# Kernel optimization log

Measured on AMD Instinct MI355X. Metric: run time of the kernel, lower is better.

The kernel has to match this reference:

```python
import jax, jax.numpy as jnp
import numpy as np

G = (1.0, 1.0)  # metric signature, n_blades = 4

def to_hypercomplex(x, n_blades):
    # (..., n_blades*C) -> (..., C, n_blades)
    return x.reshape(*x.shape[:-1], n_blades, -1).swapaxes(-2, -1)

def clifford_kernel_2d(w, g):
    # w: (4, out, in) -> kernel (4*out, 4*in), cliffordlayers get_2d_clifford_kernel
    g0, g1 = g
    k0 = jnp.concatenate([w[0],  g0 * w[1],  g1 * w[2], -g0 * g1 * w[3]], axis=1)
    k1 = jnp.concatenate([w[1],  w[0],      -g1 * w[3],  g1 * w[2]], axis=1)
    k2 = jnp.concatenate([w[2],  g0 * w[3],  w[0],      -g0 * w[1]], axis=1)
    k3 = jnp.concatenate([w[3],  w[2],       w[1],       w[0]], axis=1)
    return jnp.concatenate([k0, k1, k2, k3], axis=0)

def clifford_linear(x, w, b, g=G):
    # x: (N, C_in, 4) ; w: (4, C_out, C_in) ; b: (4, C_out)
    N = x.shape[0]
    k = clifford_kernel_2d(w, g)                      # (4*C_out, 4*C_in)
    xf = x.swapaxes(-2, -1).reshape(N, -1)            # blade-major flatten (N, 4*C_in)
    out = xf @ k.T + b.reshape(-1)                    # (N, 4*C_out)
    C_out = w.shape[1]
    return out.reshape(N, 4, C_out).swapaxes(-2, -1)  # (N, C_out, 4)

def setup_inputs() -> dict:
    key = jax.random.key(0)
    ks = jax.random.split(key, 10)
    N, E, R, emb_dim = 100000, 600000, 500, 256
    C = emb_dim // 4
    s = 0.05
    return {
        "h": jax.random.normal(ks[0], (N, emb_dim), jnp.float32),
        "edge_index": jax.random.randint(ks[1], (2, E), 0, N, jnp.int64),
        "edge_type": jax.random.randint(ks[2], (E,), 0, R, jnp.int64),
        "relation_emb": jax.random.normal(ks[3], (R, emb_dim), jnp.float32),
        "msg_w": jax.random.normal(ks[4], (4, C, C), jnp.float32) * s,
        "msg_b": jax.random.normal(ks[5], (4, C), jnp.float32) * s,
        "upd_w": jax.random.normal(ks[6], (4, C, C), jnp.float32) * s,
        "upd_b": jax.random.normal(ks[7], (4, C), jnp.float32) * s,
        "gate_w": jax.random.normal(ks[8], (1, emb_dim), jnp.float32) * s,
        "gate_b": jax.random.normal(ks[9], (1,), jnp.float32) * s,
    }

def reference(h, edge_index, edge_type, relation_emb, msg_w, msg_b, upd_w, upd_b, gate_w, gate_b):
    n_blades = 4
    num_nodes = h.shape[0]
    h_hc = to_hypercomplex(h, n_blades)               # (N, C, 4)
    r_hc = to_hypercomplex(relation_emb, n_blades)    # (R, C, 4)
    src, dst = edge_index[0], edge_index[1]
    h_src = h_hc[src]                                 # (E, C, 4)
    r_uv = r_hc[edge_type]                            # (E, C, 4)
    m = clifford_linear(h_src * r_uv, msg_w, msg_b)   # (E, C, 4)
    gate = jax.nn.sigmoid(r_uv.reshape(r_uv.shape[0], -1) @ gate_w.T + gate_b)  # (E, 1)
    m = m * gate[:, :, None]
    ones = jnp.ones_like(src, dtype=jnp.float32)
    deg_src = jax.ops.segment_sum(ones, src, num_segments=num_nodes)
    deg_dst = jax.ops.segment_sum(ones, dst, num_segments=num_nodes)
    norm = jnp.maximum(deg_src[src] * deg_dst[dst], 1.0) ** -0.5
    m = m * norm[:, None, None]
    h_agg = jax.ops.segment_sum(m, dst, num_segments=num_nodes)  # (N, C, 4)
    h_out = clifford_linear(h_hc + h_agg, upd_w, upd_b)          # (N, C, 4)
    return h_out.reshape(num_nodes, -1)
```

## Files before the change

### kernel.cpp

```cpp
#include <hip/hip_runtime.h>
#include <math.h>

typedef unsigned int u32;
typedef unsigned short u16;
typedef __attribute__((ext_vector_type(8))) short bf16x8;
typedef __attribute__((ext_vector_type(4))) float f32x4;

__device__ inline u16 f2bf(float x) {
    union { float f; u32 u; } v; v.f = x;
    u32 r = v.u + 0x7FFFu + ((v.u >> 16) & 1u);
    return (u16)(r >> 16);
}
__device__ inline float bf2f(u16 x) { return __uint_as_float((u32)x << 16); }
__device__ inline float bf_lo(u32 u) { return __uint_as_float(u << 16); }
__device__ inline float bf_hi(u32 u) { return __uint_as_float(u & 0xffff0000u); }

__device__ __forceinline__ int cs_s(int ob, int ib) { return ob ^ ib; }
__device__ __forceinline__ float cs_g(int ob, int ib) {
    return ((ob != 3) && (ib == (3 ^ (ob & 1)))) ? -1.f : 1.f;
}

#define CAP 32


template <int BF>
__global__ __launch_bounds__(256) void prepC_kernel(
    const float* __restrict__ msg_w, const float* __restrict__ upd_w,
    const float* __restrict__ upd_b, const float* __restrict__ msg_b,
    const float* __restrict__ rel_emb, const float* __restrict__ gate_w,
    const float* __restrict__ gate_b, const float* __restrict__ h,
    const int* __restrict__ ei, const int* __restrict__ et, int E,
    u32* __restrict__ deg_src, u32* __restrict__ cursor,
    u32* __restrict__ bucket,
    float* __restrict__ gate, u16* __restrict__ Kcomb,
    float* __restrict__ c0, float* __restrict__ c1,
    u16* __restrict__ h_bf, u16* __restrict__ rel_bf,
    int N, int R, int nbDeg, int nbGate, int nbRel, int nbH) {
    __shared__ __align__(16) u16 ms[16384];
    __shared__ float U_s[256];
    __shared__ float wred[4];
    int tid = threadIdx.x;
    int idx = blockIdx.x >> 1;

    if (blockIdx.x & 1) {
        if (idx < 256) {
            int p = idx;
            int j = (p & 3) * 64 + (p >> 2);
#pragma unroll
            for (int i = 0; i < 8; ++i) {
                int c8 = i * 256 + tid;
                const float* p8 = msg_w + (size_t)c8 * 8;
                float4 a = *(const float4*)(p8);
                float4 bb = *(const float4*)(p8 + 4);
                u16 tmp[8] = {f2bf(a.x), f2bf(a.y), f2bf(a.z), f2bf(a.w),
                              f2bf(bb.x), f2bf(bb.y), f2bf(bb.z), f2bf(bb.w)};
                *(uint4*)&ms[c8 * 8] = *(const uint4*)tmp;
            }
            int ib = tid >> 6, ic = tid & 63;
            {
                int obu = j >> 6;
                U_s[tid] = cs_g(obu, ib) * upd_w[cs_s(obu, ib) * 4096 + (j & 63) * 64 + ic];
            }
            __syncthreads();
            float acc = 0.f;
#pragma unroll
            for (int ob = 0; ob < 4; ++ob) {
                int s = cs_s(ob, ib);
                float gg = cs_g(ob, ib);
                const u16* mp = ms + s * 4096 + ic;
                const float* us = U_s + ob * 64;
                float a0 = 0.f;
#pragma unroll 8
                for (int oc = 0; oc < 64; ++oc) a0 += us[oc] * bf2f(mp[oc * 64]);
                acc += gg * a0;
            }
            u16 vA = f2bf(acc);
            u16 vU = f2bf(U_s[tid]);
            int pt = p >> 4, pl = p & 15;
            int kgA = (tid >> 3) & 3, elA = tid & 7;
            size_t addrA = (size_t)(pt * 16 + (tid >> 5)) * 512 + (kgA * 16 + pl) * 8 + elA;
            int ku = tid + 256;
            size_t addrU = (size_t)(pt * 16 + (ku >> 5)) * 512 + (kgA * 16 + pl) * 8 + elA;
#pragma unroll
            for (int r = 0; r < 8; ++r) {
                Kcomb[(size_t)r * 131072 + addrA] = vA;
                Kcomb[(size_t)r * 131072 + addrU] = vU;
            }
            float part = U_s[tid] * msg_b[tid];
            int lane = tid & 63, wv = tid >> 6;
#pragma unroll
            for (int d = 32; d > 0; d >>= 1) part += __shfl_down(part, d);
            if (lane == 0) wred[wv] = part;
            __syncthreads();
            if (tid == 0) { c1[p] = wred[0] + wred[1] + wred[2] + wred[3]; c0[p] = upd_b[j]; }
            return;
        }
        int gb = idx - 256;
        if (gb < nbGate) {
            int wv = tid >> 6, lane = tid & 63;
            int r = gb * 4 + wv;
            if (r >= R) return;
            float4 rv = *(const float4*)(rel_emb + (size_t)r * 256 + lane * 4);
            float s = 0.f;
            float rvv[4] = {rv.x, rv.y, rv.z, rv.w};
#pragma unroll
            for (int c = 0; c < 4; ++c) {
                int jj = lane * 4 + c;
                s += rvv[c] * gate_w[(jj & 63) * 4 + (jj >> 6)];
            }
#pragma unroll
            for (int d = 32; d > 0; d >>= 1) s += __shfl_down(s, d);
            if (lane == 0) gate[r] = 1.0f / (1.0f + expf(-(s + gate_b[0])));
            return;
        }
        int rb = gb - nbGate;
        if (BF && rb < nbRel) {
            int i = rb * 256 + tid;
            if (i < R * 32) {
                const float* p8 = rel_emb + (size_t)i * 8;
                float4 a = *(const float4*)(p8);
                float4 bb = *(const float4*)(p8 + 4);
                u16 tmp[8] = {f2bf(a.x), f2bf(a.y), f2bf(a.z), f2bf(a.w),
                              f2bf(bb.x), f2bf(bb.y), f2bf(bb.z), f2bf(bb.w)};
                *(uint4*)(rel_bf + (size_t)i * 8) = *(const uint4*)tmp;
            }
            return;
        }
        int hb = rb - nbRel;
        if (BF && hb < nbH) {
            int n8 = N * 32;
            for (int i = hb * 256 + tid; i < n8; i += nbH * 256) {
                const float* p8 = h + (size_t)i * 8;
                float4 a = *(const float4*)(p8);
                float4 bb = *(const float4*)(p8 + 4);
                u16 tmp[8] = {f2bf(a.x), f2bf(a.y), f2bf(a.z), f2bf(a.w),
                              f2bf(bb.x), f2bf(bb.y), f2bf(bb.z), f2bf(bb.w)};
                *(uint4*)(h_bf + (size_t)i * 8) = *(const uint4*)tmp;
            }
        }
        return;
    }
    if (idx < nbDeg) {
        int e = idx * 256 + tid;
        if (e < E) {
            int src = ei[e];
            int dst = ei[E + e];
            int rel = et[e];
            atomicAdd(&deg_src[src], 1u);
            u32 pos = atomicAdd(&cursor[dst], 1u);
            if (pos < CAP)
                bucket[(size_t)dst * CAP + pos] = (u32)src | ((u32)rel << 18);
        }
    }
}

template <int BF>
__global__ __launch_bounds__(256, 4) void aggemm_kernel(
    float* __restrict__ dio,
    const float* __restrict__ h, const u16* __restrict__ h_bf,
    const float* __restrict__ rel_emb, const u16* __restrict__ rel_bf,
    const u16* __restrict__ Kcomb,
    const u32* __restrict__ cursor, const u32* __restrict__ deg_src,
    const u32* __restrict__ bucket, const float* __restrict__ gate,
    const float* __restrict__ c0, const float* __restrict__ c1, int N) {
    __shared__ __align__(16) u16 xs[32 * 512];
    __shared__ float ws_l[32];
    const int lane = threadIdx.x & 63;
    const int wv = threadIdx.x >> 6;
    const int l15 = lane & 15;
    const int kg = lane >> 4;
    const int half = lane >> 5, l32 = lane & 31;
    const int m0 = blockIdx.x * 32;
    const int pbase = wv * 64;
    const int pt0 = wv * 4;
    const u16* Kr = Kcomb + (size_t)(blockIdx.x & 7) * 131072;

    u32 ns4[4];
    float ddf4[4];
    u32 ent4[4];
    uint4 hrow4[4];
#pragma unroll
    for (int rnd = 0; rnd < 4; ++rnd) {
        int m = wv * 8 + rnd * 2 + half;
        int n = m0 + m;
        bool valid = n < N;
        u32 dd = valid ? cursor[n] : 0u;
        ns4[rnd] = dd < CAP ? dd : CAP;
        ddf4[rnd] = (float)dd;
        ent4[rnd] = (valid && l32 < (int)ns4[rnd])
                        ? bucket[(size_t)n * CAP + l32] : 0u;
        uint4 hr = make_uint4(0u, 0u, 0u, 0u);
        if (valid) {
            if (BF) {
                hr = *(const uint4*)(h_bf + (size_t)n * 256 + l32 * 8);
            } else {
                const float* hp = h + (size_t)n * 256 + l32 * 8;
                float4 f0 = *(const float4*)hp, f1 = *(const float4*)(hp + 4);
                u16 tmp[8] = {f2bf(f0.x), f2bf(f0.y), f2bf(f0.z), f2bf(f0.w),
                              f2bf(f1.x), f2bf(f1.y), f2bf(f1.z), f2bf(f1.w)};
                hr = *(const uint4*)tmp;
            }
        }
        hrow4[rnd] = hr;
    }

    float w4[4];
#pragma unroll
    for (int rnd = 0; rnd < 4; ++rnd) {
        float wl = 0.f;
        if (l32 < (int)ns4[rnd]) {
            u32 src_l = ent4[rnd] & 0x3FFFFu, rel_l = ent4[rnd] >> 18;
            float ds = (float)deg_src[src_l];
            wl = gate[rel_l] * rsqrtf(fmaxf(ds * ddf4[rnd], 1.0f));
        }
        w4[rnd] = wl;
    }

#pragma unroll
    for (int rnd = 0; rnd < 4; ++rnd) {
        int m = wv * 8 + rnd * 2 + half;
        u32 ns = ns4[rnd];
        int swm = (m & 7) << 3;
        u32 ent_l = ent4[rnd];
        float w_l = w4[rnd];

        float acc[8];
#pragma unroll
        for (int j = 0; j < 8; ++j) acc[j] = 0.f;
        float wsum = 0.f;

        for (u32 e = 0; e < ns; e += 4) {
            u32 ent[4];
            float wq[4];
            uint4 hv[4], rv[4];
#pragma unroll
            for (int q = 0; q < 4; ++q) {
                u32 idxq = e + q;
                u32 cl = (idxq < ns) ? idxq : (ns - 1);
                ent[q] = __shfl(ent_l, (int)cl, 32);
                float wv_ = __shfl(w_l, (int)cl, 32);
                wq[q] = (idxq < ns) ? wv_ : 0.f;
            }
#pragma unroll
            for (int q = 0; q < 4; ++q) {
                u32 src = ent[q] & 0x3FFFFu, rel = ent[q] >> 18;
                if (BF) {
                    hv[q] = *(const uint4*)(h_bf + (size_t)src * 256 + l32 * 8);
                    rv[q] = *(const uint4*)(rel_bf + (size_t)rel * 256 + l32 * 8);
                } else {
                    const float* hp = h + (size_t)src * 256 + l32 * 8;
                    const float* rp = rel_emb + (size_t)rel * 256 + l32 * 8;
                    float4 hf0 = *(const float4*)hp, hf1 = *(const float4*)(hp + 4);
                    float4 rf0 = *(const float4*)rp, rf1 = *(const float4*)(rp + 4);
                    u16 th[8] = {f2bf(hf0.x), f2bf(hf0.y), f2bf(hf0.z), f2bf(hf0.w),
                                 f2bf(hf1.x), f2bf(hf1.y), f2bf(hf1.z), f2bf(hf1.w)};
                    u16 tr[8] = {f2bf(rf0.x), f2bf(rf0.y), f2bf(rf0.z), f2bf(rf0.w),
                                 f2bf(rf1.x), f2bf(rf1.y), f2bf(rf1.z), f2bf(rf1.w)};
                    hv[q] = *(const uint4*)th;
                    rv[q] = *(const uint4*)tr;
                }
            }
#pragma unroll
            for (int q = 0; q < 4; ++q) {
                float w = wq[q];
                u32 hu[4] = {hv[q].x, hv[q].y, hv[q].z, hv[q].w};
                u32 ru[4] = {rv[q].x, rv[q].y, rv[q].z, rv[q].w};
#pragma unroll
                for (int c = 0; c < 4; ++c) {
                    acc[c * 2 + 0] += w * bf_lo(hu[c]) * bf_lo(ru[c]);
                    acc[c * 2 + 1] += w * bf_hi(hu[c]) * bf_hi(ru[c]);
                }
                wsum += w;
            }
        }

        u32 outw[4];
#pragma unroll
        for (int c = 0; c < 4; ++c)
            outw[c] = (u32)f2bf(acc[c * 2]) | ((u32)f2bf(acc[c * 2 + 1]) << 16);
        *(uint4*)&xs[m * 512 + ((l32 * 8) ^ swm)] = *(const uint4*)outw;
        *(uint4*)&xs[m * 512 + ((256 + l32 * 8) ^ swm)] = hrow4[rnd];
        if (l32 == 0) ws_l[m] = wsum;
    }
    __syncthreads();

    f32x4 acc[2][4];
#pragma unroll
    for (int f = 0; f < 2; ++f)
#pragma unroll
        for (int nf = 0; nf < 4; ++nf) acc[f][nf] = (f32x4)(0.f);

    const int swz = (l15 & 7) << 3;
#pragma unroll 4
    for (int k0 = 0; k0 < 512; k0 += 32) {
        int kk = k0 + kg * 8;
        int ksi = k0 >> 5;
        bf16x8 a[2], b[4];
#pragma unroll
        for (int f = 0; f < 2; ++f)
            a[f] = *(const bf16x8*)&xs[(f * 16 + l15) * 512 + (kk ^ swz)];
#pragma unroll
        for (int nf = 0; nf < 4; ++nf)
            b[nf] = *(const bf16x8*)(Kr + (size_t)((pt0 + nf) * 16 + ksi) * 512 + lane * 8);
#pragma unroll
        for (int f = 0; f < 2; ++f)
#pragma unroll
            for (int nf = 0; nf < 4; ++nf)
                acc[f][nf] = __builtin_amdgcn_mfma_f32_16x16x32_bf16(a[f], b[nf], acc[f][nf], 0, 0, 0);
    }

    float b0[4], b1[4];
#pragma unroll
    for (int nf = 0; nf < 4; ++nf) {
        int p = pbase + nf * 16 + l15;
        b0[nf] = c0[p];
        b1[nf] = c1[p];
    }
#pragma unroll
    for (int f = 0; f < 2; ++f) {
#pragma unroll
        for (int r = 0; r < 4; ++r) {
            int m = f * 16 + kg * 4 + r;
            int row = m0 + m;
            if (row >= N) continue;
            float wsv = ws_l[m];
#pragma unroll
            for (int nf = 0; nf < 4; ++nf) {
                int p = pbase + nf * 16 + l15;
                dio[(size_t)row * 256 + p] = acc[f][nf][r] + b0[nf] + b1[nf] * wsv;
            }
        }
    }
}

static inline size_t align4(size_t x) { return (x + 3) & ~(size_t)3; }
static inline int imax(int a, int b) { return a > b ? a : b; }

extern "C" void kernel_launch(void* const* d_in, const int* in_sizes, int n_in,
                              void* d_out, int out_size, void* d_ws, size_t ws_size,
                              hipStream_t stream) {
    const float* h       = (const float*)d_in[0];
    const int*   ei      = (const int*)d_in[1];
    const int*   et      = (const int*)d_in[2];
    const float* rel_emb = (const float*)d_in[3];
    const float* msg_w   = (const float*)d_in[4];
    const float* msg_b   = (const float*)d_in[5];
    const float* upd_w   = (const float*)d_in[6];
    const float* upd_b   = (const float*)d_in[7];
    const float* gate_w  = (const float*)d_in[8];
    const float* gate_b  = (const float*)d_in[9];

    const int N = in_sizes[0] / 256;
    const int E = in_sizes[2];
    const int R = in_sizes[3] / 256;

    u32* ws = (u32*)d_ws;
    size_t o = 0;
    u32* deg_src  = ws + o; o += align4((size_t)N);
    u32* cursor   = ws + o; o += align4((size_t)N);
    float* gate   = (float*)(ws + o); o += align4((size_t)R);
    u32* bucket   = ws + o; o += (size_t)align4((size_t)N) * CAP;
    u16* Kcomb    = (u16*)(ws + o); o += 524288;
    float* c0     = (float*)(ws + o); o += 256;
    float* c1     = (float*)(ws + o); o += 256;
    size_t need_base = o;
    u16* h_bf     = (u16*)(ws + o); o += (size_t)N * 128;
    u16* rel_bf   = (u16*)(ws + o); o += (size_t)R * 128;
    size_t need_bf = o;

    if (ws_size < need_base * 4) return;
    const bool use_bf = (ws_size >= need_bf * 4);

    float* out = (float*)d_out;

    hipMemsetAsync(deg_src, 0, 2 * align4((size_t)N) * 4, stream);

    const int nbDeg  = (E + 255) / 256;
    const int nbGate = (R + 3) / 4;
    const int nbRel  = use_bf ? (R * 32 + 255) / 256 : 0;
    const int nbH    = use_bf ? imax(256, nbDeg - 256 - nbGate - nbRel) : 0;
    const int gridC  = 2 * imax(nbDeg, 256 + nbGate + nbRel + nbH);
    if (use_bf) {
        prepC_kernel<1><<<gridC, 256, 0, stream>>>(
            msg_w, upd_w, upd_b, msg_b, rel_emb, gate_w, gate_b, h, ei, et, E,
            deg_src, cursor, bucket, gate, Kcomb, c0, c1, h_bf, rel_bf,
            N, R, nbDeg, nbGate, nbRel, nbH);
        aggemm_kernel<1><<<(N + 31) / 32, 256, 0, stream>>>(
            out, h, h_bf, rel_emb, rel_bf, Kcomb, cursor, deg_src, bucket, gate,
            c0, c1, N);
    } else {
        prepC_kernel<0><<<gridC, 256, 0, stream>>>(
            msg_w, upd_w, upd_b, msg_b, rel_emb, gate_w, gate_b, h, ei, et, E,
            deg_src, cursor, bucket, gate, Kcomb, c0, c1, h_bf, rel_bf,
            N, R, nbDeg, nbGate, nbRel, nbH);
        aggemm_kernel<0><<<(N + 31) / 32, 256, 0, stream>>>(
            out, h, h_bf, rel_emb, rel_bf, Kcomb, cursor, deg_src, bucket, gate,
            c0, c1, N);
    }
}
```

Baseline: 177.1 us.

## Load self-node A operand directly from global, halving shared staging

Stops staging each node's own h row in shared memory alongside the aggregated messages. The second half of the K loop now reads the h operand straight from global memory (bf16 or converted from fp32) into MFMA registers. This halves the LDS buffer and drops the hrow registers, and the occupancy target is raised from 4 to 6 blocks per CU. In exchange, every wave reloads the h rows from global/L2 instead of sharing one LDS copy, and the 6-wave launch bound may squeeze registers.

```diff
diff --git a/kernel.cpp b/kernel.cpp
--- a/kernel.cpp
+++ b/kernel.cpp
@@ -155,7 +155,7 @@
 }
 
 template <int BF>
-__global__ __launch_bounds__(256, 4) void aggemm_kernel(
+__global__ __launch_bounds__(256, 6) void aggemm_kernel(
     float* __restrict__ dio,
     const float* __restrict__ h, const u16* __restrict__ h_bf,
     const float* __restrict__ rel_emb, const u16* __restrict__ rel_bf,
@@ -163,7 +163,7 @@
     const u32* __restrict__ cursor, const u32* __restrict__ deg_src,
     const u32* __restrict__ bucket, const float* __restrict__ gate,
     const float* __restrict__ c0, const float* __restrict__ c1, int N) {
-    __shared__ __align__(16) u16 xs[32 * 512];
+    __shared__ __align__(16) u16 xs[32 * 256];
     __shared__ float ws_l[32];
     const int lane = threadIdx.x & 63;
     const int wv = threadIdx.x >> 6;
@@ -178,7 +178,6 @@
     u32 ns4[4];
     float ddf4[4];
     u32 ent4[4];
-    uint4 hrow4[4];
 #pragma unroll
     for (int rnd = 0; rnd < 4; ++rnd) {
         int m = wv * 8 + rnd * 2 + half;
@@ -189,19 +188,6 @@
         ddf4[rnd] = (float)dd;
         ent4[rnd] = (valid && l32 < (int)ns4[rnd])
                         ? bucket[(size_t)n * CAP + l32] : 0u;
-        uint4 hr = make_uint4(0u, 0u, 0u, 0u);
-        if (valid) {
-            if (BF) {
-                hr = *(const uint4*)(h_bf + (size_t)n * 256 + l32 * 8);
-            } else {
-                const float* hp = h + (size_t)n * 256 + l32 * 8;
-                float4 f0 = *(const float4*)hp, f1 = *(const float4*)(hp + 4);
-                u16 tmp[8] = {f2bf(f0.x), f2bf(f0.y), f2bf(f0.z), f2bf(f0.w),
-                              f2bf(f1.x), f2bf(f1.y), f2bf(f1.z), f2bf(f1.w)};
-                hr = *(const uint4*)tmp;
-            }
-        }
-        hrow4[rnd] = hr;
     }
 
     float w4[4];
@@ -278,8 +264,7 @@
 #pragma unroll
         for (int c = 0; c < 4; ++c)
             outw[c] = (u32)f2bf(acc[c * 2]) | ((u32)f2bf(acc[c * 2 + 1]) << 16);
-        *(uint4*)&xs[m * 512 + ((l32 * 8) ^ swm)] = *(const uint4*)outw;
-        *(uint4*)&xs[m * 512 + ((256 + l32 * 8) ^ swm)] = hrow4[rnd];
+        *(uint4*)&xs[m * 256 + ((l32 * 8) ^ swm)] = *(const uint4*)outw;
         if (l32 == 0) ws_l[m] = wsum;
     }
     __syncthreads();
@@ -289,16 +274,51 @@
     for (int f = 0; f < 2; ++f)
 #pragma unroll
         for (int nf = 0; nf < 4; ++nf) acc[f][nf] = (f32x4)(0.f);
+
+    int rowA[2];
+#pragma unroll
+    for (int f = 0; f < 2; ++f) {
+        int r = m0 + f * 16 + l15;
+        rowA[f] = (r < N) ? r : (N - 1);
+    }
 
     const int swz = (l15 & 7) << 3;
 #pragma unroll 4
-    for (int k0 = 0; k0 < 512; k0 += 32) {
+    for (int k0 = 0; k0 < 256; k0 += 32) {
         int kk = k0 + kg * 8;
         int ksi = k0 >> 5;
         bf16x8 a[2], b[4];
 #pragma unroll
         for (int f = 0; f < 2; ++f)
-            a[f] = *(const bf16x8*)&xs[(f * 16 + l15) * 512 + (kk ^ swz)];
+            a[f] = *(const bf16x8*)&xs[(f * 16 + l15) * 256 + (kk ^ swz)];
+#pragma unroll
+        for (int nf = 0; nf < 4; ++nf)
+            b[nf] = *(const bf16x8*)(Kr + (size_t)((pt0 + nf) * 16 + ksi) * 512 + lane * 8);
+#pragma unroll
+        for (int f = 0; f < 2; ++f)
+#pragma unroll
+            for (int nf = 0; nf < 4; ++nf)
+                acc[f][nf] = __builtin_amdgcn_mfma_f32_16x16x32_bf16(a[f], b[nf], acc[f][nf], 0, 0, 0);
+    }
+#pragma unroll 4
+    for (int k0 = 256; k0 < 512; k0 += 32) {
+        int kh = (k0 - 256) + kg * 8;
+        int ksi = k0 >> 5;
+        bf16x8 a[2], b[4];
+        if (BF) {
+#pragma unroll
+            for (int f = 0; f < 2; ++f)
+                a[f] = *(const bf16x8*)(h_bf + (size_t)rowA[f] * 256 + kh);
+        } else {
+#pragma unroll
+            for (int f = 0; f < 2; ++f) {
+                const float* hp = h + (size_t)rowA[f] * 256 + kh;
+                float4 f0 = *(const float4*)hp, f1 = *(const float4*)(hp + 4);
+                u16 tmp[8] = {f2bf(f0.x), f2bf(f0.y), f2bf(f0.z), f2bf(f0.w),
+                              f2bf(f1.x), f2bf(f1.y), f2bf(f1.z), f2bf(f1.w)};
+                a[f] = *(const bf16x8*)tmp;
+            }
+        }
 #pragma unroll
         for (int nf = 0; nf < 4; ++nf)
             b[nf] = *(const bf16x8*)(Kr + (size_t)((pt0 + nf) * 16 + ksi) * 512 + lane * 8);
```

New measurement: 191.4 us. +8.0%, slower.

## Split aggregation-GEMM block across 8 waves instead of 4

Applied to the files above, without the earlier changes.

Doubles the block size of the fused aggregate+GEMM kernel to 512 threads. Each wave now gathers 4 node rows instead of 8, and in the GEMM computes one 16-row tile per column group instead of two. This halves per-wave serial gather latency and register use (launch bounds raised to 512, 8) to expose more parallelism. The cost is that each B fragment from Kcomb is reloaded by twice as many waves, adding global/L2 traffic.

```diff
diff --git a/kernel.cpp b/kernel.cpp
--- a/kernel.cpp
+++ b/kernel.cpp
@@ -155,7 +155,7 @@
 }
 
 template <int BF>
-__global__ __launch_bounds__(256, 4) void aggemm_kernel(
+__global__ __launch_bounds__(512, 8) void aggemm_kernel(
     float* __restrict__ dio,
     const float* __restrict__ h, const u16* __restrict__ h_bf,
     const float* __restrict__ rel_emb, const u16* __restrict__ rel_bf,
@@ -171,17 +171,19 @@
     const int kg = lane >> 4;
     const int half = lane >> 5, l32 = lane & 31;
     const int m0 = blockIdx.x * 32;
-    const int pbase = wv * 64;
-    const int pt0 = wv * 4;
+    const int rg = wv >> 2;
+    const int cg = wv & 3;
+    const int pbase = cg * 64;
+    const int pt0 = cg * 4;
     const u16* Kr = Kcomb + (size_t)(blockIdx.x & 7) * 131072;
 
-    u32 ns4[4];
-    float ddf4[4];
-    u32 ent4[4];
-    uint4 hrow4[4];
-#pragma unroll
-    for (int rnd = 0; rnd < 4; ++rnd) {
-        int m = wv * 8 + rnd * 2 + half;
+    u32 ns4[2];
+    float ddf4[2];
+    u32 ent4[2];
+    uint4 hrow4[2];
+#pragma unroll
+    for (int rnd = 0; rnd < 2; ++rnd) {
+        int m = wv * 4 + rnd * 2 + half;
         int n = m0 + m;
         bool valid = n < N;
         u32 dd = valid ? cursor[n] : 0u;
@@ -204,9 +206,9 @@
         hrow4[rnd] = hr;
     }
 
-    float w4[4];
-#pragma unroll
-    for (int rnd = 0; rnd < 4; ++rnd) {
+    float w4[2];
+#pragma unroll
+    for (int rnd = 0; rnd < 2; ++rnd) {
         float wl = 0.f;
         if (l32 < (int)ns4[rnd]) {
             u32 src_l = ent4[rnd] & 0x3FFFFu, rel_l = ent4[rnd] >> 18;
@@ -217,8 +219,8 @@
     }
 
 #pragma unroll
-    for (int rnd = 0; rnd < 4; ++rnd) {
-        int m = wv * 8 + rnd * 2 + half;
+    for (int rnd = 0; rnd < 2; ++rnd) {
+        int m = wv * 4 + rnd * 2 + half;
         u32 ns = ns4[rnd];
         int swm = (m & 7) << 3;
         u32 ent_l = ent4[rnd];
@@ -284,51 +286,36 @@
     }
     __syncthreads();
 
-    f32x4 acc[2][4];
-#pragma unroll
-    for (int f = 0; f < 2; ++f)
-#pragma unroll
-        for (int nf = 0; nf < 4; ++nf) acc[f][nf] = (f32x4)(0.f);
+    f32x4 acc[4];
+#pragma unroll
+    for (int nf = 0; nf < 4; ++nf) acc[nf] = (f32x4)(0.f);
 
     const int swz = (l15 & 7) << 3;
 #pragma unroll 4
     for (int k0 = 0; k0 < 512; k0 += 32) {
         int kk = k0 + kg * 8;
         int ksi = k0 >> 5;
-        bf16x8 a[2], b[4];
-#pragma unroll
-        for (int f = 0; f < 2; ++f)
-            a[f] = *(const bf16x8*)&xs[(f * 16 + l15) * 512 + (kk ^ swz)];
+        bf16x8 a = *(const bf16x8*)&xs[(rg * 16 + l15) * 512 + (kk ^ swz)];
+        bf16x8 b[4];
 #pragma unroll
         for (int nf = 0; nf < 4; ++nf)
             b[nf] = *(const bf16x8*)(Kr + (size_t)((pt0 + nf) * 16 + ksi) * 512 + lane * 8);
 #pragma unroll
-        for (int f = 0; f < 2; ++f)
-#pragma unroll
-            for (int nf = 0; nf < 4; ++nf)
-                acc[f][nf] = __builtin_amdgcn_mfma_f32_16x16x32_bf16(a[f], b[nf], acc[f][nf], 0, 0, 0);
-    }
-
-    float b0[4], b1[4];
+        for (int nf = 0; nf < 4; ++nf)
+            acc[nf] = __builtin_amdgcn_mfma_f32_16x16x32_bf16(a, b[nf], acc[nf], 0, 0, 0);
+    }
+
 #pragma unroll
     for (int nf = 0; nf < 4; ++nf) {
         int p = pbase + nf * 16 + l15;
-        b0[nf] = c0[p];
-        b1[nf] = c1[p];
-    }
-#pragma unroll
-    for (int f = 0; f < 2; ++f) {
+        float b0 = c0[p];
+        float b1 = c1[p];
 #pragma unroll
         for (int r = 0; r < 4; ++r) {
-            int m = f * 16 + kg * 4 + r;
+            int m = rg * 16 + kg * 4 + r;
             int row = m0 + m;
-            if (row >= N) continue;
-            float wsv = ws_l[m];
-#pragma unroll
-            for (int nf = 0; nf < 4; ++nf) {
-                int p = pbase + nf * 16 + l15;
-                dio[(size_t)row * 256 + p] = acc[f][nf][r] + b0[nf] + b1[nf] * wsv;
-            }
+            if (row < N)
+                dio[(size_t)row * 256 + p] = acc[nf][r] + b0 + b1 * ws_l[m];
         }
     }
 }
@@ -385,7 +372,7 @@
             msg_w, upd_w, upd_b, msg_b, rel_emb, gate_w, gate_b, h, ei, et, E,
             deg_src, cursor, bucket, gate, Kcomb, c0, c1, h_bf, rel_bf,
             N, R, nbDeg, nbGate, nbRel, nbH);
-        aggemm_kernel<1><<<(N + 31) / 32, 256, 0, stream>>>(
+        aggemm_kernel<1><<<(N + 31) / 32, 512, 0, stream>>>(
             out, h, h_bf, rel_emb, rel_bf, Kcomb, cursor, deg_src, bucket, gate,
             c0, c1, N);
     } else {
@@ -393,7 +380,7 @@
             msg_w, upd_w, upd_b, msg_b, rel_emb, gate_w, gate_b, h, ei, et, E,
             deg_src, cursor, bucket, gate, Kcomb, c0, c1, h_bf, rel_bf,
             N, R, nbDeg, nbGate, nbRel, nbH);
-        aggemm_kernel<0><<<(N + 31) / 32, 256, 0, stream>>>(
+        aggemm_kernel<0><<<(N + 31) / 32, 512, 0, stream>>>(
             out, h, h_bf, rel_emb, rel_bf, Kcomb, cursor, deg_src, bucket, gate,
             c0, c1, N);
     }
```

After: 220.2 us. 24.3% more time.
